# Performance work log

Hardware: AMD Instinct MI355X
Metric: run time of the kernel (lower is better)

Reference implementation:

```python
import jax, jax.numpy as jnp
import numpy as np

N_NODES = 50000
N_EDGES = 500000
HIDDEN = 128
HEADS = 8
HEAD_DIM = HIDDEN // HEADS
EPS = 1e-16  # PyG softmax denominator epsilon


def _kaiming(key, shape):
    fan_in = shape[0]
    return jax.random.normal(key, shape, dtype=jnp.float32) * np.sqrt(2.0 / fan_in)


def prelu(x, a):
    return jnp.maximum(x, 0.0) + a * jnp.minimum(x, 0.0)


def transformer_conv(x, src, dst, Wq, bq, Wk, bk, Wv, bv, Ws, bs):
    """PyG TransformerConv (concat=True, root_weight=True, beta=False), eval mode."""
    N = x.shape[0]
    q = (x @ Wq + bq).reshape(N, HEADS, HEAD_DIM)
    k = (x @ Wk + bk).reshape(N, HEADS, HEAD_DIM)
    v = (x @ Wv + bv).reshape(N, HEADS, HEAD_DIM)
    # per-edge attention: query from destination, key/value from source
    score = jnp.einsum('ehd,ehd->eh', q[dst], k[src]) / np.sqrt(HEAD_DIM)  # [E,H]
    m = jax.ops.segment_max(score, dst, num_segments=N)                     # [N,H]
    e = jnp.exp(score - m[dst])
    s = jax.ops.segment_sum(e, dst, num_segments=N)
    alpha = e / (s[dst] + EPS)                                              # [E,H]
    agg = jax.ops.segment_sum(alpha[..., None] * v[src], dst, num_segments=N)
    return agg.reshape(N, HIDDEN) + x @ Ws + bs  # skip connection (lin_skip)


def setup_inputs() -> dict:
    key = jax.random.key(0)
    ks = jax.random.split(key, 12)
    inp = {
        'x': jax.random.normal(ks[0], (N_NODES, HIDDEN), dtype=jnp.float32),
        'edge_index': jax.random.randint(ks[1], (2, N_EDGES), 0, N_NODES, dtype=jnp.int64 if jax.config.jax_enable_x64 else jnp.int32),
        'prelu_w': jnp.full((1,), 0.25, dtype=jnp.float32),
    }
    i = 2
    for layer in (1, 2):
        for nm in ('q', 'k', 'v', 's'):
            inp[f'W{nm}{layer}'] = _kaiming(ks[i], (HIDDEN, HIDDEN))
            inp[f'b{nm}{layer}'] = jnp.zeros((HIDDEN,), dtype=jnp.float32)
            i += 1
        ks = jax.random.split(ks[-1], 12)
        i = 0
    return inp


def reference(x, edge_index, prelu_w,
              Wq1, bq1, Wk1, bk1, Wv1, bv1, Ws1, bs1,
              Wq2, bq2, Wk2, bk2, Wv2, bv2, Ws2, bs2):
    src, dst = edge_index[0], edge_index[1]
    o = transformer_conv(x, src, dst, Wq1, bq1, Wk1, bk1, Wv1, bv1, Ws1, bs1)
    o = prelu(o, prelu_w)
    o = transformer_conv(o, src, dst, Wq2, bq2, Wk2, bk2, Wv2, bv2, Ws2, bs2)
    o = o + x  # residual
    return prelu(o, prelu_w)
```

## Files before the change

### kernel.cpp

```cpp
#include <hip/hip_runtime.h>

#define NN 50000
#define NE 500000
#define HID 128
#define MT 782

typedef __attribute__((ext_vector_type(8))) short short8;
typedef __attribute__((ext_vector_type(8))) _Float16 half8;
typedef __attribute__((ext_vector_type(2))) _Float16 half2v;
typedef __attribute__((ext_vector_type(4))) float f32x4;
typedef unsigned short ushort_t;
typedef unsigned int uint32;
typedef _Float16 half_t;

__device__ __forceinline__ ushort_t f2h(float f) {
    union { half_t h; ushort_t u; } x; x.h = (half_t)f; return x.u;
}
__device__ __forceinline__ half2v u2h2(uint32 u) {
    union { uint32 u; half2v h; } x; x.u = u; return x.h;
}

__global__ void pack_w2(const float* __restrict__ Wq1, const float* __restrict__ Wk1,
                        const float* __restrict__ Wv1, const float* __restrict__ Ws1,
                        const float* __restrict__ Wq2, const float* __restrict__ Wk2,
                        const float* __restrict__ Wv2, const float* __restrict__ Ws2,
                        ushort_t* __restrict__ Bt1, ushort_t* __restrict__ Bt2)
{
    int idx = blockIdx.x * 256 + threadIdx.x;
    int layer = idx >> 16;
    int r = idx & 65535;
    int col = r >> 7;
    int kk = r & 127;
    int wsel = col >> 7;
    const float* W = (layer == 0)
        ? ((wsel == 0) ? Wq1 : (wsel == 1) ? Wk1 : (wsel == 2) ? Wv1 : Ws1)
        : ((wsel == 0) ? Wq2 : (wsel == 1) ? Wk2 : (wsel == 2) ? Wv2 : Ws2);
    float val = W[kk * HID + (col & 127)];
    if (wsel == 0) val *= 0.25f;
    (layer == 0 ? Bt1 : Bt2)[r] = f2h(val);
}

template <int LAYER>
__global__ __launch_bounds__(256, 5) void gemm_mfma(
    const float* __restrict__ Xf, const ushort_t* __restrict__ Xh,
    const ushort_t* __restrict__ Bt,
    const float* __restrict__ bqp, const float* __restrict__ bkp,
    const float* __restrict__ bvp, const float* __restrict__ bsp,
    ushort_t* __restrict__ Qb, ushort_t* __restrict__ KVb, ushort_t* __restrict__ Sfb)
{
    __shared__ ushort_t As[64 * 128];
    __shared__ ushort_t Bs[64 * 128];
    const int wgid = blockIdx.x;
    const int xcd = wgid & 7, kidx = wgid >> 3;
    const int local = xcd * MT + kidx;
    const int mtile = local >> 3;
    const int gg = local & 7;
    const int g = gg >> 1;
    const int colbase = (gg & 1) * 64;
    const int Mbase = mtile * 64;
    const int tid = threadIdx.x;
    const int lane = tid & 63, wave = tid >> 6;

    #pragma unroll
    for (int it = 0; it < 4; ++it) {
        int lin = it * 256 + tid;
        int row = lin >> 4, s = lin & 15;
        int rg = Mbase + row; if (rg >= NN) rg = NN - 1;
        short8 v;
        if (LAYER == 1) {
            float4 f0 = *reinterpret_cast<const float4*>(Xf + (size_t)rg * HID + s * 8);
            float4 f1 = *reinterpret_cast<const float4*>(Xf + (size_t)rg * HID + s * 8 + 4);
            v[0] = (short)f2h(f0.x); v[1] = (short)f2h(f0.y);
            v[2] = (short)f2h(f0.z); v[3] = (short)f2h(f0.w);
            v[4] = (short)f2h(f1.x); v[5] = (short)f2h(f1.y);
            v[6] = (short)f2h(f1.z); v[7] = (short)f2h(f1.w);
        } else {
            v = *reinterpret_cast<const short8*>(Xh + (size_t)rg * HID + s * 8);
        }
        *reinterpret_cast<short8*>((char*)As + row * 256 + ((s * 16) ^ ((row & 7) * 16))) = v;
    }
    #pragma unroll
    for (int it = 0; it < 4; ++it) {
        int lin = it * 256 + tid;
        int col = lin >> 4, s = lin & 15;
        short8 v = *reinterpret_cast<const short8*>(
            Bt + (size_t)(g * 128 + colbase + col) * HID + s * 8);
        *reinterpret_cast<short8*>((char*)Bs + col * 256 + ((s * 16) ^ ((col & 7) * 16))) = v;
    }
    __syncthreads();

    const int l15 = lane & 15;
    const int wrow = wave * 16;
    f32x4 acc[4] = {};
    #pragma unroll
    for (int kk = 0; kk < 4; ++kk) {
        int kbyte = kk * 64 + (lane >> 4) * 16;
        int ar = wrow + l15;
        half8 a = *reinterpret_cast<const half8*>(
            (const char*)As + ar * 256 + (kbyte ^ ((ar & 7) * 16)));
        #pragma unroll
        for (int nb = 0; nb < 4; ++nb) {
            int c = nb * 16 + l15;
            half8 b = *reinterpret_cast<const half8*>(
                (const char*)Bs + c * 256 + (kbyte ^ ((c & 7) * 16)));
            acc[nb] = __builtin_amdgcn_mfma_f32_16x16x32_f16(a, b, acc[nb], 0, 0, 0);
        }
    }
    __syncthreads();

    const float* bias = (g == 0) ? bqp : (g == 1) ? bkp : (g == 2) ? bvp : bsp;
    float* Cs = reinterpret_cast<float*>(As);
    #pragma unroll
    for (int nb = 0; nb < 4; ++nb) {
        int c = nb * 16 + l15;
        float bb = bias[colbase + c];
        if (g == 0) bb *= 0.25f;
        #pragma unroll
        for (int r = 0; r < 4; ++r) {
            int rl = wrow + (lane >> 4) * 4 + r;
            Cs[rl * 64 + c] = acc[nb][r] + bb;
        }
    }
    __syncthreads();

    #pragma unroll
    for (int it = 0; it < 2; ++it) {
        int lin = it * 256 + tid;
        int row = lin >> 3, s = lin & 7;
        int rg = Mbase + row;
        if (rg < NN) {
            float4 v0 = *reinterpret_cast<float4*>(&Cs[row * 64 + s * 8]);
            float4 v1 = *reinterpret_cast<float4*>(&Cs[row * 64 + s * 8 + 4]);
            short8 o;
            o[0] = (short)f2h(v0.x); o[1] = (short)f2h(v0.y);
            o[2] = (short)f2h(v0.z); o[3] = (short)f2h(v0.w);
            o[4] = (short)f2h(v1.x); o[5] = (short)f2h(v1.y);
            o[6] = (short)f2h(v1.z); o[7] = (short)f2h(v1.w);
            ushort_t* dst = (g == 0) ? (Qb  + (size_t)rg * HID + colbase + s * 8)
                          : (g == 1) ? (KVb + (size_t)rg * 256 + colbase + s * 8)
                          : (g == 2) ? (KVb + (size_t)rg * 256 + 128 + colbase + s * 8)
                          :            (Sfb + (size_t)rg * HID + colbase + s * 8);
            *reinterpret_cast<short8*>(dst) = o;
        }
    }
}

__global__ void zero_i32(int* __restrict__ p, int n)
{
    int i = blockIdx.x * blockDim.x + threadIdx.x;
    if (i < n) p[i] = 0;
}

__global__ void hist_kernel(const int* __restrict__ dst, int* __restrict__ counts)
{
    int e = blockIdx.x * blockDim.x + threadIdx.x;
    if (e < NE) atomicAdd(&counts[dst[e]], 1);
}

#define SCAN_B 196

__global__ __launch_bounds__(256) void block_sums(const int* __restrict__ counts,
                                                  int* __restrict__ bsum)
{
    int i = blockIdx.x * 256 + threadIdx.x;
    int v = (i < NN) ? counts[i] : 0;
    #pragma unroll
    for (int o = 1; o < 64; o <<= 1) v += __shfl_xor(v, o);
    __shared__ int ws[4];
    if ((threadIdx.x & 63) == 0) ws[threadIdx.x >> 6] = v;
    __syncthreads();
    if (threadIdx.x == 0) bsum[blockIdx.x] = ws[0] + ws[1] + ws[2] + ws[3];
}

__global__ __launch_bounds__(256) void scan_bsums(const int* __restrict__ bsum,
                                                  int* __restrict__ bbase)
{
    __shared__ int sh[256];
    int t = threadIdx.x;
    int v = (t < SCAN_B) ? bsum[t] : 0;
    sh[t] = v;
    __syncthreads();
    for (int o = 1; o < 256; o <<= 1) {
        int u = (t >= o) ? sh[t - o] : 0;
        __syncthreads();
        sh[t] += u;
        __syncthreads();
    }
    bbase[t] = (t > 0) ? sh[t - 1] : 0;
}

__global__ __launch_bounds__(256) void write_offsets(const int* __restrict__ counts,
        const int* __restrict__ bbase, int* __restrict__ offsets, int* __restrict__ cursor)
{
    __shared__ int sh[256];
    int t = threadIdx.x;
    int i = blockIdx.x * 256 + t;
    int v = (i < NN) ? counts[i] : 0;
    sh[t] = v;
    __syncthreads();
    for (int o = 1; o < 256; o <<= 1) {
        int u = (t >= o) ? sh[t - o] : 0;
        __syncthreads();
        sh[t] += u;
        __syncthreads();
    }
    int excl = sh[t] - v + bbase[blockIdx.x];
    if (i < NN) { offsets[i] = excl; cursor[i] = excl; }
    if (i == NN - 1) offsets[NN] = excl + v;
}

__global__ void scatter_kernel(const int* __restrict__ src, const int* __restrict__ dst,
                               int* __restrict__ cursor, int* __restrict__ csr_src)
{
    int e = blockIdx.x * blockDim.x + threadIdx.x;
    if (e < NE) {
        int pos = atomicAdd(&cursor[dst[e]], 1);
        csr_src[pos] = src[e];
    }
}

template <int LAYER>
__global__ __launch_bounds__(256) void edge_aggregate(
    const half_t* __restrict__ Qh, const half_t* __restrict__ KVh,
    const half_t* __restrict__ Sh,
    const int* __restrict__ offsets, const int* __restrict__ csr_src,
    const float* __restrict__ xres, const float* __restrict__ prelu_w,
    float* __restrict__ outF, ushort_t* __restrict__ outH)
{
    const int lane = threadIdx.x & 63;
    const int wid  = __builtin_amdgcn_readfirstlane((int)(threadIdx.x >> 6));
    const int node = blockIdx.x * 4 + wid;
    const bool hi  = lane >= 32;
    const int  c   = lane & 31;

    uint2 qu = *reinterpret_cast<const uint2*>(Qh + (size_t)node * HID + c * 4);
    half2v qa = u2h2(qu.x), qb = u2h2(qu.y);
    const float q0 = (float)qa[0], q1 = (float)qa[1];
    const float q2 = (float)qb[0], q3 = (float)qb[1];

    const int beg = offsets[node];
    const int end = offsets[node + 1];

    float den = 0.f, a0 = 0.f, a1 = 0.f, a2 = 0.f, a3 = 0.f;

#define COMPUTE(KU, VU) {                                                      \
        half2v k01 = u2h2((KU).x), k23 = u2h2((KU).y);                         \
        float p = (float)k01[0] * q0 + (float)k01[1] * q1                      \
                + (float)k23[0] * q2 + (float)k23[1] * q3;                     \
        p += __shfl_xor(p, 1); p += __shfl_xor(p, 2);                          \
        float w = __expf(p);                                                   \
        den += w;                                                              \
        half2v v01 = u2h2((VU).x), v23 = u2h2((VU).y);                         \
        a0 += w * (float)v01[0]; a1 += w * (float)v01[1];                      \
        a2 += w * (float)v23[0]; a3 += w * (float)v23[1]; }

    int i = beg;
    for (; i + 8 <= end; i += 8) {
        uint2 ku[4], vu[4];
        #pragma unroll
        for (int j = 0; j < 4; ++j) {
            int s = hi ? csr_src[i + 2 * j + 1] : csr_src[i + 2 * j];
            const half_t* kv = KVh + (size_t)s * 256 + c * 4;
            ku[j] = *reinterpret_cast<const uint2*>(kv);
            vu[j] = *reinterpret_cast<const uint2*>(kv + 128);
        }
        #pragma unroll
        for (int j = 0; j < 4; ++j) COMPUTE(ku[j], vu[j])
    }
    for (; i + 2 <= end; i += 2) {
        int s = hi ? csr_src[i + 1] : csr_src[i];
        const half_t* kv = KVh + (size_t)s * 256 + c * 4;
        uint2 ku = *reinterpret_cast<const uint2*>(kv);
        uint2 vu = *reinterpret_cast<const uint2*>(kv + 128);
        COMPUTE(ku, vu)
    }
    if (i < end) {
        int s = csr_src[i];
        const half_t* kv = KVh + (size_t)s * 256 + c * 4;
        uint2 ku = *reinterpret_cast<const uint2*>(kv);
        uint2 vu = *reinterpret_cast<const uint2*>(kv + 128);
        half2v k01 = u2h2(ku.x), k23 = u2h2(ku.y);
        float p = (float)k01[0] * q0 + (float)k01[1] * q1
                + (float)k23[0] * q2 + (float)k23[1] * q3;
        p += __shfl_xor(p, 1); p += __shfl_xor(p, 2);
        float w = hi ? 0.f : __expf(p);
        den += w;
        half2v v01 = u2h2(vu.x), v23 = u2h2(vu.y);
        a0 += w * (float)v01[0]; a1 += w * (float)v01[1];
        a2 += w * (float)v23[0]; a3 += w * (float)v23[1];
    }
#undef COMPUTE

    den += __shfl_xor(den, 32);
    a0 += __shfl_xor(a0, 32); a1 += __shfl_xor(a1, 32);
    a2 += __shfl_xor(a2, 32); a3 += __shfl_xor(a3, 32);

    if (!hi) {
        float inv = (den > 0.f) ? 1.f / den : 0.f;
        uint2 su = *reinterpret_cast<const uint2*>(Sh + (size_t)node * HID + c * 4);
        half2v s01 = u2h2(su.x), s23 = u2h2(su.y);
        float r0 = a0 * inv + (float)s01[0];
        float r1 = a1 * inv + (float)s01[1];
        float r2 = a2 * inv + (float)s23[0];
        float r3 = a3 * inv + (float)s23[1];
        if (LAYER == 2) {
            float4 xr = *reinterpret_cast<const float4*>(xres + (size_t)node * HID + c * 4);
            r0 += xr.x; r1 += xr.y; r2 += xr.z; r3 += xr.w;
        }
        const float al = prelu_w[0];
        r0 = fmaxf(r0, 0.f) + al * fminf(r0, 0.f);
        r1 = fmaxf(r1, 0.f) + al * fminf(r1, 0.f);
        r2 = fmaxf(r2, 0.f) + al * fminf(r2, 0.f);
        r3 = fmaxf(r3, 0.f) + al * fminf(r3, 0.f);
        if (LAYER == 1) {
            uint2 o;
            o.x = (uint32)f2h(r0) | ((uint32)f2h(r1) << 16);
            o.y = (uint32)f2h(r2) | ((uint32)f2h(r3) << 16);
            *reinterpret_cast<uint2*>(outH + (size_t)node * HID + c * 4) = o;
        } else {
            float4 o; o.x = r0; o.y = r1; o.z = r2; o.w = r3;
            *reinterpret_cast<float4*>(outF + (size_t)node * HID + c * 4) = o;
        }
    }
}

extern "C" void kernel_launch(void* const* d_in, const int* in_sizes, int n_in,
                              void* d_out, int out_size, void* d_ws, size_t ws_size,
                              hipStream_t stream)
{
    const float* x       = (const float*)d_in[0];
    const int*   ei      = (const int*)d_in[1];
    const float* prelu_w = (const float*)d_in[2];
    const float* Wq1 = (const float*)d_in[3],  *bq1 = (const float*)d_in[4];
    const float* Wk1 = (const float*)d_in[5],  *bk1 = (const float*)d_in[6];
    const float* Wv1 = (const float*)d_in[7],  *bv1 = (const float*)d_in[8];
    const float* Ws1 = (const float*)d_in[9],  *bs1 = (const float*)d_in[10];
    const float* Wq2 = (const float*)d_in[11], *bq2 = (const float*)d_in[12];
    const float* Wk2 = (const float*)d_in[13], *bk2 = (const float*)d_in[14];
    const float* Wv2 = (const float*)d_in[15], *bv2 = (const float*)d_in[16];
    const float* Ws2 = (const float*)d_in[17], *bs2 = (const float*)d_in[18];

    char* w = (char*)d_ws;
    size_t off = 0;
    auto alloc = [&](size_t bytes) { void* p = w + off; off += (bytes + 255) & ~(size_t)255; return p; };
    ushort_t* x1h  = (ushort_t*)alloc((size_t)NN * HID * 2);
    ushort_t* Qb   = (ushort_t*)alloc((size_t)NN * HID * 2);
    ushort_t* KVb  = (ushort_t*)alloc((size_t)NN * 256 * 2);
    ushort_t* Sfb  = (ushort_t*)alloc((size_t)NN * HID * 2);
    ushort_t* Bt1  = (ushort_t*)alloc((size_t)512 * 128 * 2);
    ushort_t* Bt2  = (ushort_t*)alloc((size_t)512 * 128 * 2);
    int* counts  = (int*)alloc(NN * sizeof(int));
    int* bsum    = (int*)alloc(256 * sizeof(int));
    int* bbase   = (int*)alloc(256 * sizeof(int));
    int* offsets = (int*)alloc((NN + 1) * sizeof(int));
    int* cursor  = (int*)alloc(NN * sizeof(int));
    int* csr_src = (int*)alloc(NE * sizeof(int));
    (void)ws_size; (void)in_sizes; (void)n_in; (void)out_size;

    const int* srcIdx = ei;
    const int* dstIdx = ei + NE;

    zero_i32<<<(NN + 255) / 256, 256, 0, stream>>>(counts, NN);
    hist_kernel<<<(NE + 255) / 256, 256, 0, stream>>>(dstIdx, counts);
    block_sums<<<SCAN_B, 256, 0, stream>>>(counts, bsum);
    scan_bsums<<<1, 256, 0, stream>>>(bsum, bbase);
    write_offsets<<<SCAN_B, 256, 0, stream>>>(counts, bbase, offsets, cursor);
    scatter_kernel<<<(NE + 255) / 256, 256, 0, stream>>>(srcIdx, dstIdx, cursor, csr_src);

    pack_w2<<<512, 256, 0, stream>>>(Wq1, Wk1, Wv1, Ws1, Wq2, Wk2, Wv2, Ws2, Bt1, Bt2);

    const int ggemm = 8 * MT;

    gemm_mfma<1><<<ggemm, 256, 0, stream>>>(x, nullptr, Bt1, bq1, bk1, bv1, bs1,
                                            Qb, KVb, Sfb);
    edge_aggregate<1><<<NN / 4, 256, 0, stream>>>((const half_t*)Qb, (const half_t*)KVb,
                                                  (const half_t*)Sfb, offsets, csr_src,
                                                  nullptr, prelu_w, nullptr, x1h);
    gemm_mfma<2><<<ggemm, 256, 0, stream>>>(nullptr, x1h, Bt2, bq2, bk2, bv2, bs2,
                                            Qb, KVb, Sfb);
    edge_aggregate<2><<<NN / 4, 256, 0, stream>>>((const half_t*)Qb, (const half_t*)KVb,
                                                  (const half_t*)Sfb, offsets, csr_src,
                                                  x, prelu_w, (float*)d_out, nullptr);
}
```

Baseline: 204.9 us.

## Bucket CSR edges by source range within each destination for locality

```diff
diff --git a/kernel.cpp b/kernel.cpp
--- a/kernel.cpp
+++ b/kernel.cpp
@@ -4,6 +4,10 @@
 #define NE 500000
 #define HID 128
 #define MT 782
+#define NP 13
+#define PSHIFT 12
+#define NBUCK (NN * NP)
+#define SCAN13_B ((NBUCK + 255) / 256)
 
 typedef __attribute__((ext_vector_type(8))) short short8;
 typedef __attribute__((ext_vector_type(8))) _Float16 half8;
@@ -145,25 +149,21 @@
     }
 }
 
-__global__ void zero_i32(int* __restrict__ p, int n)
-{
-    int i = blockIdx.x * blockDim.x + threadIdx.x;
-    if (i < n) p[i] = 0;
-}
-
-__global__ void hist_kernel(const int* __restrict__ dst, int* __restrict__ counts)
+__global__ void hist13(const int* __restrict__ src, const int* __restrict__ dst,
+                       int* __restrict__ counts8)
 {
     int e = blockIdx.x * blockDim.x + threadIdx.x;
-    if (e < NE) atomicAdd(&counts[dst[e]], 1);
-}
-
-#define SCAN_B 196
-
-__global__ __launch_bounds__(256) void block_sums(const int* __restrict__ counts,
-                                                  int* __restrict__ bsum)
+    if (e < NE) {
+        int p = src[e] >> PSHIFT;
+        atomicAdd(&counts8[dst[e] * NP + p], 1);
+    }
+}
+
+__global__ __launch_bounds__(256) void block_sums13(const int* __restrict__ counts8,
+                                                    int* __restrict__ bsum)
 {
     int i = blockIdx.x * 256 + threadIdx.x;
-    int v = (i < NN) ? counts[i] : 0;
+    int v = (i < NBUCK) ? counts8[i] : 0;
     #pragma unroll
     for (int o = 1; o < 64; o <<= 1) v += __shfl_xor(v, o);
     __shared__ int ws[4];
@@ -172,12 +172,41 @@
     if (threadIdx.x == 0) bsum[blockIdx.x] = ws[0] + ws[1] + ws[2] + ws[3];
 }
 
-__global__ __launch_bounds__(256) void scan_bsums(const int* __restrict__ bsum,
-                                                  int* __restrict__ bbase)
+__global__ __launch_bounds__(1024) void scan_bsums13(const int* __restrict__ bsum,
+                                                     int* __restrict__ bbase)
+{
+    __shared__ int sh[1024];
+    int t = threadIdx.x;
+    const int chunk = (SCAN13_B + 1023) / 1024;
+    int s = 0;
+    #pragma unroll
+    for (int j = 0; j < chunk; ++j) {
+        int i = t * chunk + j;
+        if (i < SCAN13_B) s += bsum[i];
+    }
+    sh[t] = s;
+    __syncthreads();
+    for (int o = 1; o < 1024; o <<= 1) {
+        int u = (t >= o) ? sh[t - o] : 0;
+        __syncthreads();
+        sh[t] += u;
+        __syncthreads();
+    }
+    int run = (t > 0) ? sh[t - 1] : 0;
+    #pragma unroll
+    for (int j = 0; j < chunk; ++j) {
+        int i = t * chunk + j;
+        if (i < SCAN13_B) { bbase[i] = run; run += bsum[i]; }
+    }
+}
+
+__global__ __launch_bounds__(256) void write_offsets13(const int* __restrict__ counts8,
+        const int* __restrict__ bbase, int* __restrict__ off8, int* __restrict__ cursor8)
 {
     __shared__ int sh[256];
     int t = threadIdx.x;
-    int v = (t < SCAN_B) ? bsum[t] : 0;
+    int i = blockIdx.x * 256 + t;
+    int v = (i < NBUCK) ? counts8[i] : 0;
     sh[t] = v;
     __syncthreads();
     for (int o = 1; o < 256; o <<= 1) {
@@ -186,36 +215,19 @@
         sh[t] += u;
         __syncthreads();
     }
-    bbase[t] = (t > 0) ? sh[t - 1] : 0;
-}
-
-__global__ __launch_bounds__(256) void write_offsets(const int* __restrict__ counts,
-        const int* __restrict__ bbase, int* __restrict__ offsets, int* __restrict__ cursor)
-{
-    __shared__ int sh[256];
-    int t = threadIdx.x;
-    int i = blockIdx.x * 256 + t;
-    int v = (i < NN) ? counts[i] : 0;
-    sh[t] = v;
-    __syncthreads();
-    for (int o = 1; o < 256; o <<= 1) {
-        int u = (t >= o) ? sh[t - o] : 0;
-        __syncthreads();
-        sh[t] += u;
-        __syncthreads();
-    }
     int excl = sh[t] - v + bbase[blockIdx.x];
-    if (i < NN) { offsets[i] = excl; cursor[i] = excl; }
-    if (i == NN - 1) offsets[NN] = excl + v;
-}
-
-__global__ void scatter_kernel(const int* __restrict__ src, const int* __restrict__ dst,
-                               int* __restrict__ cursor, int* __restrict__ csr_src)
+    if (i < NBUCK) { off8[i] = excl; cursor8[i] = excl; }
+    if (i == NBUCK - 1) off8[NBUCK] = excl + v;
+}
+
+__global__ void scatter13(const int* __restrict__ src, const int* __restrict__ dst,
+                          int* __restrict__ cursor8, int* __restrict__ csr_src)
 {
     int e = blockIdx.x * blockDim.x + threadIdx.x;
     if (e < NE) {
-        int pos = atomicAdd(&cursor[dst[e]], 1);
-        csr_src[pos] = src[e];
+        int s = src[e];
+        int pos = atomicAdd(&cursor8[dst[e] * NP + (s >> PSHIFT)], 1);
+        csr_src[pos] = s;
     }
 }
 
@@ -223,7 +235,7 @@
 __global__ __launch_bounds__(256) void edge_aggregate(
     const half_t* __restrict__ Qh, const half_t* __restrict__ KVh,
     const half_t* __restrict__ Sh,
-    const int* __restrict__ offsets, const int* __restrict__ csr_src,
+    const int* __restrict__ off8, const int* __restrict__ csr_src,
     const float* __restrict__ xres, const float* __restrict__ prelu_w,
     float* __restrict__ outF, ushort_t* __restrict__ outH)
 {
@@ -238,8 +250,8 @@
     const float q0 = (float)qa[0], q1 = (float)qa[1];
     const float q2 = (float)qb[0], q3 = (float)qb[1];
 
-    const int beg = offsets[node];
-    const int end = offsets[node + 1];
+    const int beg = off8[node * NP];
+    const int end = off8[node * NP + NP];
 
     float den = 0.f, a0 = 0.f, a1 = 0.f, a2 = 0.f, a3 = 0.f;
 
@@ -349,23 +361,23 @@
     ushort_t* Sfb  = (ushort_t*)alloc((size_t)NN * HID * 2);
     ushort_t* Bt1  = (ushort_t*)alloc((size_t)512 * 128 * 2);
     ushort_t* Bt2  = (ushort_t*)alloc((size_t)512 * 128 * 2);
-    int* counts  = (int*)alloc(NN * sizeof(int));
-    int* bsum    = (int*)alloc(256 * sizeof(int));
-    int* bbase   = (int*)alloc(256 * sizeof(int));
-    int* offsets = (int*)alloc((NN + 1) * sizeof(int));
-    int* cursor  = (int*)alloc(NN * sizeof(int));
+    int* counts8 = (int*)alloc((size_t)NBUCK * sizeof(int));
+    int* bsum    = (int*)alloc(SCAN13_B * sizeof(int));
+    int* bbase   = (int*)alloc(SCAN13_B * sizeof(int));
+    int* off8    = (int*)alloc(((size_t)NBUCK + 1) * sizeof(int));
+    int* cursor8 = (int*)alloc((size_t)NBUCK * sizeof(int));
     int* csr_src = (int*)alloc(NE * sizeof(int));
     (void)ws_size; (void)in_sizes; (void)n_in; (void)out_size;
 
     const int* srcIdx = ei;
     const int* dstIdx = ei + NE;
 
-    zero_i32<<<(NN + 255) / 256, 256, 0, stream>>>(counts, NN);
-    hist_kernel<<<(NE + 255) / 256, 256, 0, stream>>>(dstIdx, counts);
-    block_sums<<<SCAN_B, 256, 0, stream>>>(counts, bsum);
-    scan_bsums<<<1, 256, 0, stream>>>(bsum, bbase);
-    write_offsets<<<SCAN_B, 256, 0, stream>>>(counts, bbase, offsets, cursor);
-    scatter_kernel<<<(NE + 255) / 256, 256, 0, stream>>>(srcIdx, dstIdx, cursor, csr_src);
+    hipMemsetAsync(counts8, 0, (size_t)NBUCK * sizeof(int), stream);
+    hist13<<<(NE + 255) / 256, 256, 0, stream>>>(srcIdx, dstIdx, counts8);
+    block_sums13<<<SCAN13_B, 256, 0, stream>>>(counts8, bsum);
+    scan_bsums13<<<1, 1024, 0, stream>>>(bsum, bbase);
+    write_offsets13<<<SCAN13_B, 256, 0, stream>>>(counts8, bbase, off8, cursor8);
+    scatter13<<<(NE + 255) / 256, 256, 0, stream>>>(srcIdx, dstIdx, cursor8, csr_src);
 
     pack_w2<<<512, 256, 0, stream>>>(Wq1, Wk1, Wv1, Ws1, Wq2, Wk2, Wv2, Ws2, Bt1, Bt2);
 
@@ -374,11 +386,11 @@
     gemm_mfma<1><<<ggemm, 256, 0, stream>>>(x, nullptr, Bt1, bq1, bk1, bv1, bs1,
                                             Qb, KVb, Sfb);
     edge_aggregate<1><<<NN / 4, 256, 0, stream>>>((const half_t*)Qb, (const half_t*)KVb,
-                                                  (const half_t*)Sfb, offsets, csr_src,
+                                                  (const half_t*)Sfb, off8, csr_src,
                                                   nullptr, prelu_w, nullptr, x1h);
     gemm_mfma<2><<<ggemm, 256, 0, stream>>>(nullptr, x1h, Bt2, bq2, bk2, bv2, bs2,
                                             Qb, KVb, Sfb);
     edge_aggregate<2><<<NN / 4, 256, 0, stream>>>((const half_t*)Qb, (const half_t*)KVb,
-                                                  (const half_t*)Sfb, offsets, csr_src,
+                                                  (const half_t*)Sfb, off8, csr_src,
                                                   x, prelu_w, (float*)d_out, nullptr);
 }
```

Result: no change. 205.9 us (+0.5%).
